# Kernel tuning notes

Measured on AMD Instinct MI355X. Metric: run time of the kernel, lower is better.

Reference implementation:

```python
import jax, jax.numpy as jnp
import numpy as np

V, E, H, N, T = 2000, 256, 256, 4096, 16


def lstm_scan(x_seq, W_ih, W_hh, b, h0, c0):
    # x_seq: [T, B, D]; PyTorch gate order i, f, g, o
    def step(carry, x_t):
        h, c = carry
        gates = x_t @ W_ih.T + h @ W_hh.T + b  # [B, 4H]
        i, f, g, o = jnp.split(gates, 4, axis=-1)
        c = jax.nn.sigmoid(f) * c + jax.nn.sigmoid(i) * jnp.tanh(g)
        h = jax.nn.sigmoid(o) * jnp.tanh(c)
        return (h, c), h
    (hT, cT), hs = jax.lax.scan(step, (h0, c0), x_seq)
    return hs, hT


def setup_inputs() -> dict:
    key = jax.random.key(0)
    ks = jax.random.split(key, 12)
    s = float(1.0 / np.sqrt(H))
    u = lambda k, shape: jax.random.uniform(k, shape, jnp.float32, -s, s)
    return {
        "token_ids": jax.random.randint(ks[0], (N, T), 0, V),
        "lengths": jax.random.randint(ks[1], (N,), 1, T + 1),
        "emb": jax.random.normal(ks[2], (V, E), jnp.float32),
        "tok_W_ih": u(ks[3], (4 * H, E)),
        "tok_W_hh": u(ks[4], (4 * H, H)),
        "tok_b": u(ks[5], (4 * H,)),  # b_ih + b_hh fused
        "ins_W_ih": u(ks[6], (4 * H, H)),
        "ins_W_hh": u(ks[7], (4 * H, H)),
        "ins_b": u(ks[8], (4 * H,)),
        "lin_W": u(ks[9], (1, H)),
        "lin_b": u(ks[10], (1,)),
    }


def reference(token_ids, lengths, emb, tok_W_ih, tok_W_hh, tok_b,
              ins_W_ih, ins_W_hh, ins_b, lin_W, lin_b):
    n, t = token_ids.shape
    h = tok_W_hh.shape[1]
    x = emb[token_ids]                      # [N, T, E]
    x = jnp.transpose(x, (1, 0, 2))         # [T, N, E]
    z = jnp.zeros((n, h), x.dtype)
    hs, _ = lstm_scan(x, tok_W_ih, tok_W_hh, tok_b, z, z)   # [T, N, H]
    # last valid token output per instruction (padding doesn't affect earlier steps)
    instr_feats = hs[lengths - 1, jnp.arange(n)]            # [N, H]
    z1 = jnp.zeros((1, h), x.dtype)
    _, hT = lstm_scan(instr_feats[:, None, :], ins_W_ih, ins_W_hh, ins_b, z1, z1)  # [1, H]
    out = hT[0] @ lin_W.T + lin_b           # [1]
    return out[0]                           # scalar, matching .squeeze()


if __name__ == "__main__":
    print(reference(**setup_inputs()))
```

## Files before the change

kernel.cpp:

```cpp
#include <hip/hip_runtime.h>

#define SWEEPS 6
#define HSTRIDE 4112
#define WROW 140
#define WTSZ (8 * 256 * WROW)

__device__ __forceinline__ float sig_(float x) { return 1.0f / (1.0f + __expf(-x)); }
__device__ __forceinline__ float th_(float x)  { return 1.0f - 2.0f / (__expf(2.0f * x) + 1.0f); }

__device__ __forceinline__ void gload_lds16(const float* g, float* l) {
    __builtin_amdgcn_global_load_lds(
        (const __attribute__((address_space(1))) unsigned*)g,
        (__attribute__((address_space(3))) unsigned*)l, 16, 0, 0);
}

__global__ __launch_bounds__(256)
void wtrans(const float* __restrict__ W, float* __restrict__ WT, int ilv)
{
    __shared__ float s[32 * WROW];
    const int tid = threadIdx.x;
    const int k0 = blockIdx.x * 32;
    const int rt = blockIdx.y;
    #pragma unroll
    for (int p = 0; p < 4; ++p) {
        int idx = tid + p * 256;
        int rl = idx >> 3, k4 = idx & 7;
        int row = ilv ? ((rl & 3) * 256 + rt * 32 + (rl >> 2))
                      : (rt * 128 + rl);
        float4 v = *(const float4*)&W[row * 256 + k0 + k4 * 4];
        int pc = rl + ((rl >> 5) << 2);
        s[(k4 * 4 + 0) * WROW + pc] = v.x;
        s[(k4 * 4 + 1) * WROW + pc] = v.y;
        s[(k4 * 4 + 2) * WROW + pc] = v.z;
        s[(k4 * 4 + 3) * WROW + pc] = v.w;
    }
    __syncthreads();
    float* dst = WT + (size_t)(rt * 256 + k0) * WROW;
    for (int i = tid; i < 32 * WROW; i += 256) dst[i] = s[i];
}

__global__ __launch_bounds__(256, 2)
void gemm_emb2(const float* __restrict__ A, const float* __restrict__ Wt,
               const float* __restrict__ bias, float* __restrict__ Cout, int M)
{
    __shared__ float a_lds[32][68];
    __shared__ float b_lds[32][68];
    const int tid = threadIdx.x;
    const int tn = tid & 15;
    const int th = tid >> 4;
    const int m0 = blockIdx.x * 64;
    const int j0 = blockIdx.y * 64;

    float acc[4][4];
    #pragma unroll
    for (int x = 0; x < 4; ++x)
        #pragma unroll
        for (int y = 0; y < 4; ++y) acc[x][y] = 0.f;

    float4 abuf[2], bbuf[2];
    auto load_t = [&](int k0) {
        #pragma unroll
        for (int p = 0; p < 2; ++p) {
            int idx = tid + p * 256, ml = idx >> 3, k4 = idx & 7;
            int row = m0 + ml;
            abuf[p] = (row < M) ? *(const float4*)&A[row * 256 + k0 + k4 * 4]
                                : make_float4(0.f, 0.f, 0.f, 0.f);
            bbuf[p] = *(const float4*)&Wt[(j0 + ml) * 256 + k0 + k4 * 4];
        }
    };
    auto store_t = [&]() {
        #pragma unroll
        for (int p = 0; p < 2; ++p) {
            int idx = tid + p * 256, ml = idx >> 3, k4 = idx & 7;
            a_lds[k4 * 4 + 0][ml] = abuf[p].x;
            a_lds[k4 * 4 + 1][ml] = abuf[p].y;
            a_lds[k4 * 4 + 2][ml] = abuf[p].z;
            a_lds[k4 * 4 + 3][ml] = abuf[p].w;
            b_lds[k4 * 4 + 0][ml] = bbuf[p].x;
            b_lds[k4 * 4 + 1][ml] = bbuf[p].y;
            b_lds[k4 * 4 + 2][ml] = bbuf[p].z;
            b_lds[k4 * 4 + 3][ml] = bbuf[p].w;
        }
    };

    load_t(0); store_t(); __syncthreads();
    for (int c = 0; c < 8; ++c) {
        if (c < 7) load_t((c + 1) * 32);
        #pragma unroll 8
        for (int k = 0; k < 32; ++k) {
            float4 a4 = *(const float4*)&a_lds[k][tn * 4];
            float4 b4 = *(const float4*)&b_lds[k][th * 4];
            float av[4] = {a4.x, a4.y, a4.z, a4.w};
            float bv[4] = {b4.x, b4.y, b4.z, b4.w};
            #pragma unroll
            for (int mi = 0; mi < 4; ++mi)
                #pragma unroll
                for (int ji = 0; ji < 4; ++ji)
                    acc[mi][ji] += av[mi] * bv[ji];
        }
        __syncthreads();
        if (c < 7) { store_t(); __syncthreads(); }
    }

    const int jcol = j0 + th * 4;
    float4 bs = *(const float4*)&bias[jcol];
    #pragma unroll
    for (int mi = 0; mi < 4; ++mi) {
        int row = m0 + tn * 4 + mi;
        if (row < M) {
            float4 o;
            o.x = acc[mi][0] + bs.x;
            o.y = acc[mi][1] + bs.y;
            o.z = acc[mi][2] + bs.z;
            o.w = acc[mi][3] + bs.w;
            *(float4*)&Cout[row * 1024 + jcol] = o;
        }
    }
}

__global__ __launch_bounds__(256)
void sortlen(const int* __restrict__ len, int* __restrict__ perm,
             int* __restrict__ actcnt)
{
    __shared__ int cnt[17], off[17];
    const int tid = threadIdx.x;
    if (tid < 17) cnt[tid] = 0;
    __syncthreads();
    for (int n = tid; n < 4096; n += 256) atomicAdd(&cnt[len[n]], 1);
    __syncthreads();
    if (tid == 0) {
        int run = 0;
        for (int L = 16; L >= 1; --L) { off[L] = run; run += cnt[L]; }
        actcnt[16] = 0;
        for (int t = 1; t < 16; ++t) actcnt[t] = off[t];
        actcnt[0] = 4096;
    }
    __syncthreads();
    for (int n = tid; n < 4096; n += 256) {
        int pos = atomicAdd(&off[len[n]], 1);
        perm[pos] = n;
    }
}

__global__ __launch_bounds__(256)
void step0T(const int* __restrict__ tok, const int* __restrict__ perm,
            const int* __restrict__ actcnt, const float* __restrict__ emb2,
            float* __restrict__ cT, float* __restrict__ hT0,
            float* __restrict__ featsT)
{
    const int tid = threadIdx.x;
    const int tn = tid & 15, tu = tid >> 4;
    const int u  = blockIdx.y * 16 + tu;
    const int n0 = blockIdx.x * 64 + tn * 4;
    const int a1 = actcnt[1];
    int4 pn = *(const int4*)&perm[n0];
    const int pns[4] = {pn.x, pn.y, pn.z, pn.w};
    float h4[4], c4[4];
    #pragma unroll
    for (int j = 0; j < 4; ++j) {
        int v = tok[pns[j] * 16];
        const float* e = emb2 + v * 1024 + u;
        float ig = e[0], gg = e[512], og = e[768];
        float c = sig_(ig) * th_(gg);
        float h = sig_(og) * th_(c);
        c4[j] = c; h4[j] = h;
        if (n0 + j >= a1) featsT[u * 4096 + pns[j]] = h;
    }
    *(float4*)&cT[u * 4096 + n0]  = make_float4(c4[0], c4[1], c4[2], c4[3]);
    *(float4*)&hT0[u * 4096 + n0] = make_float4(h4[0], h4[1], h4[2], h4[3]);
}

__global__ __launch_bounds__(256, 2)
void stepT(const float* __restrict__ WT, const float* __restrict__ hTprev,
           const int* __restrict__ tok, int t, const float* __restrict__ emb2,
           const int* __restrict__ perm, const int* __restrict__ actcnt,
           float* __restrict__ cT, float* __restrict__ hTnext,
           float* __restrict__ featsT)
{
    const int s0 = blockIdx.x * 64;
    const int a_t  = actcnt[t];
    if (s0 >= a_t) return;
    const int a_t1 = actcnt[t + 1];

    __shared__ float w_lds[2][32 * WROW];
    __shared__ float h_lds[2][32][64];
    const int tid = threadIdx.x;
    const int tr = tid & 15;
    const int ts = tid >> 4;
    const int ub = blockIdx.y;
    const int scol = s0 + ts * 4;
    const int wphys = tr * 8 + ((tr >> 2) << 2);

    int4 pn = *(const int4*)&perm[scol];
    const int pns[4] = {pn.x, pn.y, pn.z, pn.w};
    int vids[4];
    #pragma unroll
    for (int j = 0; j < 4; ++j) vids[j] = tok[pns[j] * 16 + t];

    float acc[8][4];
    #pragma unroll
    for (int x = 0; x < 8; ++x)
        #pragma unroll
        for (int y = 0; y < 4; ++y) acc[x][y] = 0.f;

    auto issue_w = [&](int c, int b) {
        const float* src = WT + (size_t)(ub * 256 + c * 32) * WROW;
        #pragma unroll
        for (int p = 0; p < 4; ++p) {
            int idx = tid + p * 256;
            gload_lds16(src + idx * 4, &w_lds[b][idx * 4]);
        }
        if (tid < 96) {
            int idx = 1024 + tid;
            gload_lds16(src + idx * 4, &w_lds[b][idx * 4]);
        }
    };
    auto issue_h = [&](int k0, int b) {
        #pragma unroll
        for (int p = 0; p < 2; ++p) {
            int idx = tid + p * 256;
            int jj = idx >> 4, s4 = idx & 15;
            gload_lds16(&hTprev[(k0 + jj) * 4096 + s0 + s4 * 4],
                        &h_lds[b][jj][s4 * 4]);
        }
    };

    issue_w(0, 0); issue_h(0, 0); __syncthreads();
    for (int c = 0; c < 8; ++c) {
        const int b = c & 1;
        if (c < 7) { issue_w(c + 1, b ^ 1); issue_h((c + 1) * 32, b ^ 1); }
        #pragma unroll 4
        for (int k = 0; k < 32; ++k) {
            float4 w0 = *(const float4*)&w_lds[b][k * WROW + wphys];
            float4 w1 = *(const float4*)&w_lds[b][k * WROW + wphys + 4];
            float4 hv = *(const float4*)&h_lds[b][k][ts * 4];
            float wa[8] = {w0.x, w0.y, w0.z, w0.w, w1.x, w1.y, w1.z, w1.w};
            float ha[4] = {hv.x, hv.y, hv.z, hv.w};
            #pragma unroll
            for (int ri = 0; ri < 8; ++ri)
                #pragma unroll
                for (int si = 0; si < 4; ++si)
                    acc[ri][si] += wa[ri] * ha[si];
        }
        __syncthreads();
    }

    #pragma unroll
    for (int half = 0; half < 2; ++half) {
        const int u = ub * 32 + tr * 2 + half;
        float4 cold = *(const float4*)&cT[u * 4096 + scol];
        const float* coldp = (const float*)&cold;
        float c4[4], h4[4];
        #pragma unroll
        for (int j = 0; j < 4; ++j) {
            const float* e = emb2 + vids[j] * 1024 + u;
            float ig = acc[half * 4 + 0][j] + e[0];
            float fg = acc[half * 4 + 1][j] + e[256];
            float gg = acc[half * 4 + 2][j] + e[512];
            float og = acc[half * 4 + 3][j] + e[768];
            float cc = sig_(fg) * coldp[j] + sig_(ig) * th_(gg);
            c4[j] = cc;
            h4[j] = sig_(og) * th_(cc);
            int p = scol + j;
            if (p >= a_t1 && p < a_t)
                featsT[u * 4096 + pns[j]] = h4[j];
        }
        *(float4*)&cT[u * 4096 + scol]     = make_float4(c4[0], c4[1], c4[2], c4[3]);
        *(float4*)&hTnext[u * 4096 + scol] = make_float4(h4[0], h4[1], h4[2], h4[3]);
    }
}

__global__ __launch_bounds__(256, 2)
void gemm_T(const float* __restrict__ WT, const float* __restrict__ X, int xstride,
            const float* __restrict__ addm, const float* __restrict__ bias,
            float* __restrict__ Out)
{
    __shared__ float w_lds[2][32 * WROW];
    __shared__ float h_lds[2][32][64];
    const int tid = threadIdx.x;
    const int tr = tid & 15;
    const int ts = tid >> 4;
    const int s0 = blockIdx.x * 64;
    const int rt = blockIdx.y;
    const int wphys = tr * 8 + ((tr >> 2) << 2);

    float acc[8][4];
    #pragma unroll
    for (int x = 0; x < 8; ++x)
        #pragma unroll
        for (int y = 0; y < 4; ++y) acc[x][y] = 0.f;

    auto issue_w = [&](int c, int b) {
        const float* src = WT + (size_t)(rt * 256 + c * 32) * WROW;
        #pragma unroll
        for (int p = 0; p < 4; ++p) {
            int idx = tid + p * 256;
            gload_lds16(src + idx * 4, &w_lds[b][idx * 4]);
        }
        if (tid < 96) {
            int idx = 1024 + tid;
            gload_lds16(src + idx * 4, &w_lds[b][idx * 4]);
        }
    };
    auto issue_h = [&](int k0, int b) {
        #pragma unroll
        for (int p = 0; p < 2; ++p) {
            int idx = tid + p * 256;
            int jj = idx >> 4, s4 = idx & 15;
            gload_lds16(&X[(k0 + jj) * xstride + s0 + s4 * 4],
                        &h_lds[b][jj][s4 * 4]);
        }
    };

    issue_w(0, 0); issue_h(0, 0); __syncthreads();
    for (int c = 0; c < 8; ++c) {
        const int b = c & 1;
        if (c < 7) { issue_w(c + 1, b ^ 1); issue_h((c + 1) * 32, b ^ 1); }
        #pragma unroll 4
        for (int k = 0; k < 32; ++k) {
            float4 w0 = *(const float4*)&w_lds[b][k * WROW + wphys];
            float4 w1 = *(const float4*)&w_lds[b][k * WROW + wphys + 4];
            float4 hv = *(const float4*)&h_lds[b][k][ts * 4];
            float wa[8] = {w0.x, w0.y, w0.z, w0.w, w1.x, w1.y, w1.z, w1.w};
            float ha[4] = {hv.x, hv.y, hv.z, hv.w};
            #pragma unroll
            for (int ri = 0; ri < 8; ++ri)
                #pragma unroll
                for (int si = 0; si < 4; ++si)
                    acc[ri][si] += wa[ri] * ha[si];
        }
        __syncthreads();
    }

    const int scol = s0 + ts * 4;
    #pragma unroll
    for (int ri = 0; ri < 8; ++ri) {
        const int r = rt * 128 + tr * 8 + ri;
        float4 z;
        if (addm) {
            float4 gb = *(const float4*)&addm[r * 4096 + scol];
            z.x = acc[ri][0] + gb.x; z.y = acc[ri][1] + gb.y;
            z.z = acc[ri][2] + gb.z; z.w = acc[ri][3] + gb.w;
        } else {
            float bb = bias[r];
            z.x = acc[ri][0] + bb; z.y = acc[ri][1] + bb;
            z.z = acc[ri][2] + bb; z.w = acc[ri][3] + bb;
        }
        *(float4*)&Out[r * 4096 + scol] = z;
    }
}

__global__ __launch_bounds__(256, 1)
void scan_sweep(const float* __restrict__ ZT, float* __restrict__ hTbuf)
{
    const int u = blockIdx.x;
    const int t = threadIdx.x;
    const int s0 = t * 16;

    const float* zi = ZT + (0 * 256 + u) * 4096 + s0;
    const float* zf = ZT + (1 * 256 + u) * 4096 + s0;
    const float* zg = ZT + (2 * 256 + u) * 4096 + s0;
    const float* zo = ZT + (3 * 256 + u) * 4096 + s0;

    float4 iv[4], fv[4], gv[4], ov[4];
    #pragma unroll
    for (int p = 0; p < 4; ++p) {
        iv[p] = *(const float4*)&zi[p * 4];
        fv[p] = *(const float4*)&zf[p * 4];
        gv[p] = *(const float4*)&zg[p * 4];
        ov[p] = *(const float4*)&zo[p * 4];
    }
    float af[16], uu[16];
    const float* ivp = (const float*)iv;
    const float* fvp = (const float*)fv;
    const float* gvp = (const float*)gv;
    float A = 1.f, U = 0.f;
    #pragma unroll
    for (int k = 0; k < 16; ++k) {
        af[k] = sig_(fvp[k]);
        uu[k] = sig_(ivp[k]) * th_(gvp[k]);
        U = af[k] * U + uu[k];
        A = af[k] * A;
    }

    __shared__ float As[256], Us[256];
    As[t] = A; Us[t] = U;
    __syncthreads();
    #pragma unroll
    for (int off = 1; off < 256; off <<= 1) {
        float eA = 1.f, eU = 0.f;
        if (t >= off) { eA = As[t - off]; eU = Us[t - off]; }
        __syncthreads();
        U = A * eU + U;
        A = A * eA;
        As[t] = A; Us[t] = U;
        __syncthreads();
    }
    float c = (t > 0) ? Us[t - 1] : 0.f;

    float* hp = hTbuf + u * HSTRIDE + 1 + s0;
    const float* ovp = (const float*)ov;
    #pragma unroll
    for (int k = 0; k < 16; ++k) {
        c = af[k] * c + uu[k];
        hp[k] = sig_(ovp[k]) * th_(c);
    }
}

__global__ __launch_bounds__(256)
void out_kernel(const float* __restrict__ hTbuf, const float* __restrict__ linW,
                const float* __restrict__ linb, float* __restrict__ out)
{
    const int tid = threadIdx.x;
    __shared__ float red_lds[4];
    float p = hTbuf[tid * HSTRIDE + 4096] * linW[tid];
    #pragma unroll
    for (int off = 1; off < 64; off <<= 1) p += __shfl_xor(p, off);
    if ((tid & 63) == 0) red_lds[tid >> 6] = p;
    __syncthreads();
    if (tid == 0)
        out[0] = red_lds[0] + red_lds[1] + red_lds[2] + red_lds[3] + linb[0];
}

extern "C" void kernel_launch(void* const* d_in, const int* in_sizes, int n_in,
                              void* d_out, int out_size, void* d_ws, size_t ws_size,
                              hipStream_t stream)
{
    const int*   tok  = (const int*)d_in[0];
    const int*   len  = (const int*)d_in[1];
    const float* emb  = (const float*)d_in[2];
    const float* tWih = (const float*)d_in[3];
    const float* tWhh = (const float*)d_in[4];
    const float* tb   = (const float*)d_in[5];
    const float* iWih = (const float*)d_in[6];
    const float* iWhh = (const float*)d_in[7];
    const float* ib   = (const float*)d_in[8];
    const float* lW   = (const float*)d_in[9];
    const float* lb   = (const float*)d_in[10];
    float* out = (float*)d_out;

    float* emb2   = (float*)d_ws;
    float* hT0    = emb2   + 2048000;
    float* hT1    = hT0    + 1048576;
    float* cT     = hT1    + 1048576;
    float* featsT = cT     + 1048576;
    float* gBT    = featsT + 1048576;
    float* hTbuf  = gBT    + 4194304;
    float* tWhhT  = hTbuf  + 256 * HSTRIDE;
    float* iWhhT  = tWhhT  + WTSZ;
    float* iWihT  = iWhhT  + WTSZ;
    int*   perm   = (int*)(iWihT + WTSZ);
    int*   actcnt = perm + 4096;
    float* ZT     = hT0;

    hipMemsetAsync(hTbuf, 0, (size_t)256 * HSTRIDE * sizeof(float), stream);

    wtrans<<<dim3(8, 8), 256, 0, stream>>>(tWhh, tWhhT, 1);
    wtrans<<<dim3(8, 8), 256, 0, stream>>>(iWhh, iWhhT, 0);
    wtrans<<<dim3(8, 8), 256, 0, stream>>>(iWih, iWihT, 0);

    sortlen<<<1, 256, 0, stream>>>(len, perm, actcnt);
    gemm_emb2<<<dim3(32, 16), 256, 0, stream>>>(emb, tWih, tb, emb2, 2000);
    step0T<<<dim3(64, 16), 256, 0, stream>>>(tok, perm, actcnt, emb2, cT, hT0,
                                             featsT);
    for (int t = 1; t < 16; ++t) {
        float* hprev = (t & 1) ? hT0 : hT1;
        float* hcur  = (t & 1) ? hT1 : hT0;
        stepT<<<dim3(64, 8), 256, 0, stream>>>(tWhhT, hprev, tok, t, emb2, perm,
                                               actcnt, cT, hcur, featsT);
    }
    gemm_T<<<dim3(64, 8), 256, 0, stream>>>(iWihT, featsT, 4096, nullptr, ib, gBT);

    scan_sweep<<<256, 256, 0, stream>>>(gBT, hTbuf);
    for (int k = 1; k < SWEEPS; ++k) {
        gemm_T<<<dim3(64, 8), 256, 0, stream>>>(iWhhT, hTbuf, HSTRIDE, gBT,
                                                nullptr, ZT);
        scan_sweep<<<256, 256, 0, stream>>>(ZT, hTbuf);
    }

    out_kernel<<<1, 256, 0, stream>>>(hTbuf, lW, lb, out);
}
```

Baseline: 902.1 us.

## Fuse setup kernels, use packed FP32 FMA, swizzle LDS, skip final-step stores

Merges the three weight-transpose launches, the length sort and the hidden-buffer memset into one setup kernel. The GEMM inner loops now use inline v_pk_fma_f32 on float pairs to halve FMA instruction count, and the emb GEMM LDS tiles get an XOR swizzle to reduce bank conflicts. The shared GEMM body is factored out, and the last recurrent step skips writing c/h state that is never read. The memset now only zeros column 0 of each hTbuf row, which relies on the rest being overwritten. Inline asm op_sel choices also risk wrong lane broadcasting.

```diff
diff --git a/kernel.cpp b/kernel.cpp
--- a/kernel.cpp
+++ b/kernel.cpp
@@ -5,8 +5,19 @@
 #define WROW 140
 #define WTSZ (8 * 256 * WROW)
 
+typedef float f2 __attribute__((ext_vector_type(2)));
+
 __device__ __forceinline__ float sig_(float x) { return 1.0f / (1.0f + __expf(-x)); }
 __device__ __forceinline__ float th_(float x)  { return 1.0f - 2.0f / (__expf(2.0f * x) + 1.0f); }
+
+__device__ __forceinline__ void pk_fma_bl(f2& d, f2 a, f2 b) {
+    asm("v_pk_fma_f32 %0, %1, %2, %0 op_sel_hi:[1,0,1]"
+        : "+v"(d) : "v"(a), "v"(b));
+}
+__device__ __forceinline__ void pk_fma_bh(f2& d, f2 a, f2 b) {
+    asm("v_pk_fma_f32 %0, %1, %2, %0 op_sel:[0,1,0]"
+        : "+v"(d) : "v"(a), "v"(b));
+}
 
 __device__ __forceinline__ void gload_lds16(const float* g, float* l) {
     __builtin_amdgcn_global_load_lds(
@@ -15,47 +26,80 @@
 }
 
 __global__ __launch_bounds__(256)
-void wtrans(const float* __restrict__ W, float* __restrict__ WT, int ilv)
-{
-    __shared__ float s[32 * WROW];
-    const int tid = threadIdx.x;
-    const int k0 = blockIdx.x * 32;
-    const int rt = blockIdx.y;
-    #pragma unroll
-    for (int p = 0; p < 4; ++p) {
-        int idx = tid + p * 256;
-        int rl = idx >> 3, k4 = idx & 7;
-        int row = ilv ? ((rl & 3) * 256 + rt * 32 + (rl >> 2))
-                      : (rt * 128 + rl);
-        float4 v = *(const float4*)&W[row * 256 + k0 + k4 * 4];
-        int pc = rl + ((rl >> 5) << 2);
-        s[(k4 * 4 + 0) * WROW + pc] = v.x;
-        s[(k4 * 4 + 1) * WROW + pc] = v.y;
-        s[(k4 * 4 + 2) * WROW + pc] = v.z;
-        s[(k4 * 4 + 3) * WROW + pc] = v.w;
-    }
-    __syncthreads();
-    float* dst = WT + (size_t)(rt * 256 + k0) * WROW;
-    for (int i = tid; i < 32 * WROW; i += 256) dst[i] = s[i];
+void setup_k(const float* __restrict__ tWhh, const float* __restrict__ iWhh,
+             const float* __restrict__ iWih, float* __restrict__ tWhhT,
+             float* __restrict__ iWhhT, float* __restrict__ iWihT,
+             const int* __restrict__ len, int* __restrict__ perm,
+             int* __restrict__ actcnt, float* __restrict__ hTbuf)
+{
+    __shared__ __align__(16) float s[32 * WROW];
+    __shared__ int cnt[17], off[17];
+    const int tid = threadIdx.x;
+    const int b = blockIdx.x;
+    if (b < 192) {
+        const float* W; float* WT; int ilv;
+        if (b < 64)       { W = tWhh; WT = tWhhT; ilv = 1; }
+        else if (b < 128) { W = iWhh; WT = iWhhT; ilv = 0; }
+        else              { W = iWih; WT = iWihT; ilv = 0; }
+        const int bb = b & 63;
+        const int k0 = (bb & 7) * 32;
+        const int rt = bb >> 3;
+        #pragma unroll
+        for (int p = 0; p < 4; ++p) {
+            int idx = tid + p * 256;
+            int rl = idx >> 3, k4 = idx & 7;
+            int row = ilv ? ((rl & 3) * 256 + rt * 32 + (rl >> 2))
+                          : (rt * 128 + rl);
+            float4 v = *(const float4*)&W[row * 256 + k0 + k4 * 4];
+            int pc = rl + ((rl >> 5) << 2);
+            s[(k4 * 4 + 0) * WROW + pc] = v.x;
+            s[(k4 * 4 + 1) * WROW + pc] = v.y;
+            s[(k4 * 4 + 2) * WROW + pc] = v.z;
+            s[(k4 * 4 + 3) * WROW + pc] = v.w;
+        }
+        __syncthreads();
+        float* dst = WT + (size_t)(rt * 256 + k0) * WROW;
+        for (int i = tid; i < 32 * WROW; i += 256) dst[i] = s[i];
+    } else {
+        if (tid < 17) cnt[tid] = 0;
+        __syncthreads();
+        for (int n = tid; n < 4096; n += 256) atomicAdd(&cnt[len[n]], 1);
+        __syncthreads();
+        if (tid == 0) {
+            int run = 0;
+            for (int L = 16; L >= 1; --L) { off[L] = run; run += cnt[L]; }
+            actcnt[16] = 0;
+            for (int t = 1; t < 16; ++t) actcnt[t] = off[t];
+            actcnt[0] = 4096;
+        }
+        __syncthreads();
+        for (int n = tid; n < 4096; n += 256) {
+            int pos = atomicAdd(&off[len[n]], 1);
+            perm[pos] = n;
+        }
+        hTbuf[tid * HSTRIDE] = 0.f;
+    }
 }
 
 __global__ __launch_bounds__(256, 2)
 void gemm_emb2(const float* __restrict__ A, const float* __restrict__ Wt,
                const float* __restrict__ bias, float* __restrict__ Cout, int M)
 {
-    __shared__ float a_lds[32][68];
-    __shared__ float b_lds[32][68];
+    __shared__ float a_lds[32 * 68];
+    __shared__ float b_lds[32 * 68];
     const int tid = threadIdx.x;
     const int tn = tid & 15;
     const int th = tid >> 4;
     const int m0 = blockIdx.x * 64;
     const int j0 = blockIdx.y * 64;
 
-    float acc[4][4];
-    #pragma unroll
-    for (int x = 0; x < 4; ++x)
-        #pragma unroll
-        for (int y = 0; y < 4; ++y) acc[x][y] = 0.f;
+    f2 acc2[2][4];
+    #pragma unroll
+    for (int x = 0; x < 2; ++x)
+        #pragma unroll
+        for (int y = 0; y < 4; ++y) acc2[x][y] = f2{0.f, 0.f};
+
+    auto sw = [](int row, int col) { return col ^ (((row >> 1) & 7) << 2); };
 
     float4 abuf[2], bbuf[2];
     auto load_t = [&](int k0) {
@@ -72,14 +116,14 @@
         #pragma unroll
         for (int p = 0; p < 2; ++p) {
             int idx = tid + p * 256, ml = idx >> 3, k4 = idx & 7;
-            a_lds[k4 * 4 + 0][ml] = abuf[p].x;
-            a_lds[k4 * 4 + 1][ml] = abuf[p].y;
-            a_lds[k4 * 4 + 2][ml] = abuf[p].z;
-            a_lds[k4 * 4 + 3][ml] = abuf[p].w;
-            b_lds[k4 * 4 + 0][ml] = bbuf[p].x;
-            b_lds[k4 * 4 + 1][ml] = bbuf[p].y;
-            b_lds[k4 * 4 + 2][ml] = bbuf[p].z;
-            b_lds[k4 * 4 + 3][ml] = bbuf[p].w;
+            const float av[4] = {abuf[p].x, abuf[p].y, abuf[p].z, abuf[p].w};
+            const float bv[4] = {bbuf[p].x, bbuf[p].y, bbuf[p].z, bbuf[p].w};
+            #pragma unroll
+            for (int c = 0; c < 4; ++c) {
+                int r = k4 * 4 + c;
+                a_lds[r * 68 + sw(r, ml)] = av[c];
+                b_lds[r * 68 + sw(r, ml)] = bv[c];
+            }
         }
     };
 
@@ -88,15 +132,17 @@
         if (c < 7) load_t((c + 1) * 32);
         #pragma unroll 8
         for (int k = 0; k < 32; ++k) {
-            float4 a4 = *(const float4*)&a_lds[k][tn * 4];
-            float4 b4 = *(const float4*)&b_lds[k][th * 4];
-            float av[4] = {a4.x, a4.y, a4.z, a4.w};
-            float bv[4] = {b4.x, b4.y, b4.z, b4.w};
+            float4 a4 = *(const float4*)&a_lds[k * 68 + sw(k, tn * 4)];
+            float4 b4 = *(const float4*)&b_lds[k * 68 + sw(k, th * 4)];
+            f2 ap[2] = {f2{a4.x, a4.y}, f2{a4.z, a4.w}};
+            f2 bp[2] = {f2{b4.x, b4.y}, f2{b4.z, b4.w}};
             #pragma unroll
-            for (int mi = 0; mi < 4; ++mi)
-                #pragma unroll
-                for (int ji = 0; ji < 4; ++ji)
-                    acc[mi][ji] += av[mi] * bv[ji];
+            for (int mj = 0; mj < 2; ++mj) {
+                pk_fma_bl(acc2[mj][0], ap[mj], bp[0]);
+                pk_fma_bh(acc2[mj][1], ap[mj], bp[0]);
+                pk_fma_bl(acc2[mj][2], ap[mj], bp[1]);
+                pk_fma_bh(acc2[mj][3], ap[mj], bp[1]);
+            }
         }
         __syncthreads();
         if (c < 7) { store_t(); __syncthreads(); }
@@ -104,41 +150,18 @@
 
     const int jcol = j0 + th * 4;
     float4 bs = *(const float4*)&bias[jcol];
+    const float bsv[4] = {bs.x, bs.y, bs.z, bs.w};
     #pragma unroll
     for (int mi = 0; mi < 4; ++mi) {
         int row = m0 + tn * 4 + mi;
         if (row < M) {
-            float4 o;
-            o.x = acc[mi][0] + bs.x;
-            o.y = acc[mi][1] + bs.y;
-            o.z = acc[mi][2] + bs.z;
-            o.w = acc[mi][3] + bs.w;
-            *(float4*)&Cout[row * 1024 + jcol] = o;
-        }
-    }
-}
-
-__global__ __launch_bounds__(256)
-void sortlen(const int* __restrict__ len, int* __restrict__ perm,
-             int* __restrict__ actcnt)
-{
-    __shared__ int cnt[17], off[17];
-    const int tid = threadIdx.x;
-    if (tid < 17) cnt[tid] = 0;
-    __syncthreads();
-    for (int n = tid; n < 4096; n += 256) atomicAdd(&cnt[len[n]], 1);
-    __syncthreads();
-    if (tid == 0) {
-        int run = 0;
-        for (int L = 16; L >= 1; --L) { off[L] = run; run += cnt[L]; }
-        actcnt[16] = 0;
-        for (int t = 1; t < 16; ++t) actcnt[t] = off[t];
-        actcnt[0] = 4096;
-    }
-    __syncthreads();
-    for (int n = tid; n < 4096; n += 256) {
-        int pos = atomicAdd(&off[len[n]], 1);
-        perm[pos] = n;
+            float o[4];
+            #pragma unroll
+            for (int ji = 0; ji < 4; ++ji)
+                o[ji] = ((mi & 1) ? acc2[mi >> 1][ji].y : acc2[mi >> 1][ji].x)
+                        + bsv[ji];
+            *(float4*)&Cout[row * 1024 + jcol] = make_float4(o[0], o[1], o[2], o[3]);
+        }
     }
 }
 
@@ -170,6 +193,64 @@
     *(float4*)&hT0[u * 4096 + n0] = make_float4(h4[0], h4[1], h4[2], h4[3]);
 }
 
+__device__ __forceinline__ void gemm128x64_body(
+    int tid, float* wl, float* hl, const float* __restrict__ WT, int rt,
+    const float* __restrict__ X, int xstride, int s0, f2 acc2[4][4])
+{
+    const int tr = tid & 15;
+    const int ts = tid >> 4;
+    const int wphys = tr * 8 + ((tr >> 2) << 2);
+
+    auto issue_w = [&](int c, int b) {
+        const float* src = WT + (size_t)(rt * 256 + c * 32) * WROW;
+        float* dstb = wl + b * 4480;
+        #pragma unroll
+        for (int p = 0; p < 4; ++p) {
+            int idx = tid + p * 256;
+            gload_lds16(src + idx * 4, dstb + idx * 4);
+        }
+        if (tid < 96) {
+            int idx = 1024 + tid;
+            gload_lds16(src + idx * 4, dstb + idx * 4);
+        }
+    };
+    auto issue_h = [&](int k0, int b) {
+        float* dstb = hl + b * 2048;
+        #pragma unroll
+        for (int p = 0; p < 2; ++p) {
+            int idx = tid + p * 256;
+            int jj = idx >> 4, s4 = idx & 15;
+            gload_lds16(&X[(size_t)(k0 + jj) * xstride + s0 + s4 * 4],
+                        dstb + jj * 64 + s4 * 4);
+        }
+    };
+
+    issue_w(0, 0); issue_h(0, 0); __syncthreads();
+    for (int c = 0; c < 8; ++c) {
+        const int b = c & 1;
+        if (c < 7) { issue_w(c + 1, b ^ 1); issue_h((c + 1) * 32, b ^ 1); }
+        const float* wb = wl + b * 4480;
+        const float* hb = hl + b * 2048;
+        #pragma unroll 4
+        for (int k = 0; k < 32; ++k) {
+            float4 w0 = *(const float4*)&wb[k * WROW + wphys];
+            float4 w1 = *(const float4*)&wb[k * WROW + wphys + 4];
+            float4 hv = *(const float4*)&hb[k * 64 + ts * 4];
+            f2 wp[4] = {f2{w0.x, w0.y}, f2{w0.z, w0.w},
+                        f2{w1.x, w1.y}, f2{w1.z, w1.w}};
+            f2 hp[2] = {f2{hv.x, hv.y}, f2{hv.z, hv.w}};
+            #pragma unroll
+            for (int rj = 0; rj < 4; ++rj) {
+                pk_fma_bl(acc2[rj][0], wp[rj], hp[0]);
+                pk_fma_bh(acc2[rj][1], wp[rj], hp[0]);
+                pk_fma_bl(acc2[rj][2], wp[rj], hp[1]);
+                pk_fma_bh(acc2[rj][3], wp[rj], hp[1]);
+            }
+        }
+        __syncthreads();
+    }
+}
+
 __global__ __launch_bounds__(256, 2)
 void stepT(const float* __restrict__ WT, const float* __restrict__ hTprev,
            const int* __restrict__ tok, int t, const float* __restrict__ emb2,
@@ -182,14 +263,13 @@
     if (s0 >= a_t) return;
     const int a_t1 = actcnt[t + 1];
 
-    __shared__ float w_lds[2][32 * WROW];
-    __shared__ float h_lds[2][32][64];
+    __shared__ __align__(16) float w_lds[2 * 32 * WROW];
+    __shared__ __align__(16) float h_lds[2 * 32 * 64];
     const int tid = threadIdx.x;
     const int tr = tid & 15;
     const int ts = tid >> 4;
     const int ub = blockIdx.y;
     const int scol = s0 + ts * 4;
-    const int wphys = tr * 8 + ((tr >> 2) << 2);
 
     int4 pn = *(const int4*)&perm[scol];
     const int pns[4] = {pn.x, pn.y, pn.z, pn.w};
@@ -197,54 +277,15 @@
     #pragma unroll
     for (int j = 0; j < 4; ++j) vids[j] = tok[pns[j] * 16 + t];
 
-    float acc[8][4];
-    #pragma unroll
-    for (int x = 0; x < 8; ++x)
-        #pragma unroll
-        for (int y = 0; y < 4; ++y) acc[x][y] = 0.f;
-
-    auto issue_w = [&](int c, int b) {
-        const float* src = WT + (size_t)(ub * 256 + c * 32) * WROW;
-        #pragma unroll
-        for (int p = 0; p < 4; ++p) {
-            int idx = tid + p * 256;
-            gload_lds16(src + idx * 4, &w_lds[b][idx * 4]);
-        }
-        if (tid < 96) {
-            int idx = 1024 + tid;
-            gload_lds16(src + idx * 4, &w_lds[b][idx * 4]);
-        }
-    };
-    auto issue_h = [&](int k0, int b) {
-        #pragma unroll
-        for (int p = 0; p < 2; ++p) {
-            int idx = tid + p * 256;
-            int jj = idx >> 4, s4 = idx & 15;
-            gload_lds16(&hTprev[(k0 + jj) * 4096 + s0 + s4 * 4],
-                        &h_lds[b][jj][s4 * 4]);
-        }
-    };
-
-    issue_w(0, 0); issue_h(0, 0); __syncthreads();
-    for (int c = 0; c < 8; ++c) {
-        const int b = c & 1;
-        if (c < 7) { issue_w(c + 1, b ^ 1); issue_h((c + 1) * 32, b ^ 1); }
-        #pragma unroll 4
-        for (int k = 0; k < 32; ++k) {
-            float4 w0 = *(const float4*)&w_lds[b][k * WROW + wphys];
-            float4 w1 = *(const float4*)&w_lds[b][k * WROW + wphys + 4];
-            float4 hv = *(const float4*)&h_lds[b][k][ts * 4];
-            float wa[8] = {w0.x, w0.y, w0.z, w0.w, w1.x, w1.y, w1.z, w1.w};
-            float ha[4] = {hv.x, hv.y, hv.z, hv.w};
-            #pragma unroll
-            for (int ri = 0; ri < 8; ++ri)
-                #pragma unroll
-                for (int si = 0; si < 4; ++si)
-                    acc[ri][si] += wa[ri] * ha[si];
-        }
-        __syncthreads();
-    }
-
+    f2 acc2[4][4];
+    #pragma unroll
+    for (int x = 0; x < 4; ++x)
+        #pragma unroll
+        for (int y = 0; y < 4; ++y) acc2[x][y] = f2{0.f, 0.f};
+
+    gemm128x64_body(tid, w_lds, h_lds, WT, ub, hTprev, 4096, s0, acc2);
+
+    const bool last = (t == 15);
     #pragma unroll
     for (int half = 0; half < 2; ++half) {
         const int u = ub * 32 + tr * 2 + half;
@@ -254,10 +295,10 @@
         #pragma unroll
         for (int j = 0; j < 4; ++j) {
             const float* e = emb2 + vids[j] * 1024 + u;
-            float ig = acc[half * 4 + 0][j] + e[0];
-            float fg = acc[half * 4 + 1][j] + e[256];
-            float gg = acc[half * 4 + 2][j] + e[512];
-            float og = acc[half * 4 + 3][j] + e[768];
+            float ig = acc2[half * 2 + 0][j].x + e[0];
+            float fg = acc2[half * 2 + 0][j].y + e[256];
+            float gg = acc2[half * 2 + 1][j].x + e[512];
+            float og = acc2[half * 2 + 1][j].y + e[768];
             float cc = sig_(fg) * coldp[j] + sig_(ig) * th_(gg);
             c4[j] = cc;
             h4[j] = sig_(og) * th_(cc);
@@ -265,8 +306,10 @@
             if (p >= a_t1 && p < a_t)
                 featsT[u * 4096 + pns[j]] = h4[j];
         }
-        *(float4*)&cT[u * 4096 + scol]     = make_float4(c4[0], c4[1], c4[2], c4[3]);
-        *(float4*)&hTnext[u * 4096 + scol] = make_float4(h4[0], h4[1], h4[2], h4[3]);
+        if (!last) {
+            *(float4*)&cT[u * 4096 + scol]     = make_float4(c4[0], c4[1], c4[2], c4[3]);
+            *(float4*)&hTnext[u * 4096 + scol] = make_float4(h4[0], h4[1], h4[2], h4[3]);
+        }
     }
 }
 
@@ -275,76 +318,39 @@
             const float* __restrict__ addm, const float* __restrict__ bias,
             float* __restrict__ Out)
 {
-    __shared__ float w_lds[2][32 * WROW];
-    __shared__ float h_lds[2][32][64];
+    __shared__ __align__(16) float w_lds[2 * 32 * WROW];
+    __shared__ __align__(16) float h_lds[2 * 32 * 64];
     const int tid = threadIdx.x;
     const int tr = tid & 15;
     const int ts = tid >> 4;
     const int s0 = blockIdx.x * 64;
     const int rt = blockIdx.y;
-    const int wphys = tr * 8 + ((tr >> 2) << 2);
-
-    float acc[8][4];
-    #pragma unroll
-    for (int x = 0; x < 8; ++x)
-        #pragma unroll
-        for (int y = 0; y < 4; ++y) acc[x][y] = 0.f;
-
-    auto issue_w = [&](int c, int b) {
-        const float* src = WT + (size_t)(rt * 256 + c * 32) * WROW;
-        #pragma unroll
-        for (int p = 0; p < 4; ++p) {
-            int idx = tid + p * 256;
-            gload_lds16(src + idx * 4, &w_lds[b][idx * 4]);
-        }
-        if (tid < 96) {
-            int idx = 1024 + tid;
-            gload_lds16(src + idx * 4, &w_lds[b][idx * 4]);
-        }
-    };
-    auto issue_h = [&](int k0, int b) {
-        #pragma unroll
-        for (int p = 0; p < 2; ++p) {
-            int idx = tid + p * 256;
-            int jj = idx >> 4, s4 = idx & 15;
-            gload_lds16(&X[(k0 + jj) * xstride + s0 + s4 * 4],
-                        &h_lds[b][jj][s4 * 4]);
-        }
-    };
-
-    issue_w(0, 0); issue_h(0, 0); __syncthreads();
-    for (int c = 0; c < 8; ++c) {
-        const int b = c & 1;
-        if (c < 7) { issue_w(c + 1, b ^ 1); issue_h((c + 1) * 32, b ^ 1); }
-        #pragma unroll 4
-        for (int k = 0; k < 32; ++k) {
-            float4 w0 = *(const float4*)&w_lds[b][k * WROW + wphys];
-            float4 w1 = *(const float4*)&w_lds[b][k * WROW + wphys + 4];
-            float4 hv = *(const float4*)&h_lds[b][k][ts * 4];
-            float wa[8] = {w0.x, w0.y, w0.z, w0.w, w1.x, w1.y, w1.z, w1.w};
-            float ha[4] = {hv.x, hv.y, hv.z, hv.w};
-            #pragma unroll
-            for (int ri = 0; ri < 8; ++ri)
-                #pragma unroll
-                for (int si = 0; si < 4; ++si)
-                    acc[ri][si] += wa[ri] * ha[si];
-        }
-        __syncthreads();
-    }
+
+    f2 acc2[4][4];
+    #pragma unroll
+    for (int x = 0; x < 4; ++x)
+        #pragma unroll
+        for (int y = 0; y < 4; ++y) acc2[x][y] = f2{0.f, 0.f};
+
+    gemm128x64_body(tid, w_lds, h_lds, WT, rt, X, xstride, s0, acc2);
 
     const int scol = s0 + ts * 4;
     #pragma unroll
     for (int ri = 0; ri < 8; ++ri) {
         const int r = rt * 128 + tr * 8 + ri;
+        float a[4];
+        #pragma unroll
+        for (int si = 0; si < 4; ++si)
+            a[si] = (ri & 1) ? acc2[ri >> 1][si].y : acc2[ri >> 1][si].x;
         float4 z;
         if (addm) {
             float4 gb = *(const float4*)&addm[r * 4096 + scol];
-            z.x = acc[ri][0] + gb.x; z.y = acc[ri][1] + gb.y;
-            z.z = acc[ri][2] + gb.z; z.w = acc[ri][3] + gb.w;
+            z.x = a[0] + gb.x; z.y = a[1] + gb.y;
+            z.z = a[2] + gb.z; z.w = a[3] + gb.w;
         } else {
             float bb = bias[r];
-            z.x = acc[ri][0] + bb; z.y = acc[ri][1] + bb;
-            z.z = acc[ri][2] + bb; z.w = acc[ri][3] + bb;
+            z.x = a[0] + bb; z.y = a[1] + bb;
+            z.z = a[2] + bb; z.w = a[3] + bb;
         }
         *(float4*)&Out[r * 4096 + scol] = z;
     }
@@ -453,13 +459,9 @@
     int*   actcnt = perm + 4096;
     float* ZT     = hT0;
 
-    hipMemsetAsync(hTbuf, 0, (size_t)256 * HSTRIDE * sizeof(float), stream);
-
-    wtrans<<<dim3(8, 8), 256, 0, stream>>>(tWhh, tWhhT, 1);
-    wtrans<<<dim3(8, 8), 256, 0, stream>>>(iWhh, iWhhT, 0);
-    wtrans<<<dim3(8, 8), 256, 0, stream>>>(iWih, iWihT, 0);
-
-    sortlen<<<1, 256, 0, stream>>>(len, perm, actcnt);
+    setup_k<<<193, 256, 0, stream>>>(tWhh, iWhh, iWih, tWhhT, iWhhT, iWihT,
+                                     len, perm, actcnt, hTbuf);
+
     gemm_emb2<<<dim3(32, 16), 256, 0, stream>>>(emb, tWih, tb, emb2, 2000);
     step0T<<<dim3(64, 16), 256, 0, stream>>>(tok, perm, actcnt, emb2, cT, hT0,
                                              featsT);
```

Result: faster. 862.1 us (-4.4%).
